# Kernel optimization log

Measured on AMD Instinct MI355X. Metric: run time of the kernel, lower is better.

The kernel has to match this reference:

```python
import jax, jax.numpy as jnp
import numpy as np

V, C, H, L, BLK = 32000, 1024, 16, 4, 1024
B, T = 4, 1024
FF = 100
HD = C // H
EPS = 1e-5


def setup_inputs() -> dict:
    key = jax.random.key(0)
    ks = jax.random.split(key, 16)
    n = lambda k, s: (jax.random.normal(k, s, dtype=jnp.float32) * 0.02)
    inp = {
        "idx": jax.random.randint(ks[0], (B, T), 0, V),
        "tok_emb": n(ks[1], (V, C)),
        "pos_emb": n(ks[2], (BLK, C)),
        "Wq": n(ks[3], (L, C, C)), "bq": jnp.zeros((L, C)),
        "Wk": n(ks[4], (L, C, C)), "bk": jnp.zeros((L, C)),
        "Wv": n(ks[5], (L, C, C)), "bv": jnp.zeros((L, C)),
        "Wo": n(ks[6], (L, C, C)), "bo": jnp.zeros((L, C)),
        "ln1_w": jnp.ones((L, C)), "ln1_b": jnp.zeros((L, C)),
        "ln2_w": jnp.ones((L, C)), "ln2_b": jnp.zeros((L, C)),
        "W1": n(ks[7], (L, C, FF)), "b1": jnp.zeros((L, FF)),
        "W2": n(ks[8], (L, FF, C)), "b2": jnp.zeros((L, C)),
        "lnf_w": jnp.ones((C,)), "lnf_b": jnp.zeros((C,)),
    }
    return inp


def _ln(x, w, b):
    m = jnp.mean(x, -1, keepdims=True)
    v = jnp.mean(jnp.square(x - m), -1, keepdims=True)
    return (x - m) * jax.lax.rsqrt(v + EPS) * w + b


def reference(idx, tok_emb, pos_emb, Wq, bq, Wk, bk, Wv, bv, Wo, bo,
              ln1_w, ln1_b, ln2_w, ln2_b, W1, b1, W2, b2, lnf_w, lnf_b):
    Bn, Tn = idx.shape
    x = tok_emb[idx] + pos_emb[:Tn][None]  # [B,T,C]; dropout is identity at eval
    scale = 1.0 / np.sqrt(HD).astype(np.float32)
    att_maps = []
    for l in range(L):
        h = _ln(x, ln1_w[l], ln1_b[l])
        q = (h @ Wq[l] + bq[l]).reshape(Bn, Tn, H, HD).transpose(0, 2, 1, 3)
        k = (h @ Wk[l] + bk[l]).reshape(Bn, Tn, H, HD).transpose(0, 2, 1, 3)
        v = (h @ Wv[l] + bv[l]).reshape(Bn, Tn, H, HD).transpose(0, 2, 1, 3)
        att = jax.nn.softmax(jnp.einsum("bhqd,bhkd->bhqk", q, k) * scale, axis=-1)
        y = jnp.einsum("bhqk,bhkd->bhqd", att, v).transpose(0, 2, 1, 3).reshape(Bn, Tn, C)
        x = x + (y @ Wo[l] + bo[l])
        f = _ln(x, ln2_w[l], ln2_b[l])
        f = jax.nn.relu(f @ W1[l] + b1[l]) @ W2[l] + b2[l]
        x = x + f
        att_maps.append(att.mean(0))  # [H,T,T]
    x = _ln(x, lnf_w, lnf_b)
    pooled = x.mean(1)  # [B,C]
    return pooled, jnp.stack(att_maps)  # [L,H,T,T]
```

## Files before the change

kernel.cpp:

```cpp
#include <hip/hip_runtime.h>

typedef __bf16 bf16;
typedef __bf16 bf16x4 __attribute__((ext_vector_type(4)));
typedef __bf16 bf16x8 __attribute__((ext_vector_type(8)));
typedef float  f32x4  __attribute__((ext_vector_type(4)));

static constexpr int kC   = 1024;
static constexpr int kT   = 1024;
static constexpr int kB   = 4;
static constexpr int kH   = 16;
static constexpr int kHD  = 64;
static constexpr int kL   = 4;
static constexpr int kFF  = 100;
static constexpr int kFFP = 128;
static constexpr int kM   = kB * kT;

__device__ __forceinline__ void gload16(const bf16* g, bf16* l)
{
    __builtin_amdgcn_global_load_lds(
        (const __attribute__((address_space(1))) void*)g,
        (__attribute__((address_space(3))) void*)l, 16, 0, 0);
}

__device__ __forceinline__ unsigned bpack(float a, float b)
{
    bf16 x = (bf16)a, y = (bf16)b;
    unsigned short ux = __builtin_bit_cast(unsigned short, x);
    unsigned short uy = __builtin_bit_cast(unsigned short, y);
    return (unsigned)ux | ((unsigned)uy << 16);
}
__device__ __forceinline__ float blo(unsigned u) { return __builtin_bit_cast(float, u << 16); }
__device__ __forceinline__ float bhi(unsigned u) { return __builtin_bit_cast(float, u & 0xffff0000u); }

__global__ __launch_bounds__(256)
void prep_kernel(const float* __restrict__ Wq, const float* __restrict__ Wk,
                 const float* __restrict__ Wv, const float* __restrict__ Wo,
                 const float* __restrict__ W1, const float* __restrict__ W2,
                 const float* __restrict__ bq, const float* __restrict__ bk,
                 const float* __restrict__ bv,
                 bf16* __restrict__ WQKVT, bf16* __restrict__ WOT,
                 bf16* __restrict__ W1T, bf16* __restrict__ W2T,
                 float* __restrict__ BQKV, float* __restrict__ pooled)
{
    __shared__ float tile[32][33];
    const int bid = blockIdx.x, tid = threadIdx.x;
    const float* src; bf16* dst; int K, N, KP, NP, bx, by;
    if (bid < 12288) {
        const int slab = bid >> 10, within = bid & 1023;
        const int l = slab / 3, which = slab % 3;
        const float* W = (which == 0) ? Wq : (which == 1) ? Wk : Wv;
        src = W + (long)l * kC * kC;
        dst = WQKVT + (long)l * 3 * kC * kC + (long)which * kC * kC;
        K = N = KP = NP = kC; bx = within & 31; by = within >> 5;
    } else if (bid < 16384) {
        const int t = bid - 12288, z = t >> 10, within = t & 1023;
        src = Wo + (long)z * kC * kC; dst = WOT + (long)z * kC * kC;
        K = N = KP = NP = kC; bx = within & 31; by = within >> 5;
    } else if (bid < 16896) {
        const int t = bid - 16384, z = t >> 7, within = t & 127;
        src = W1 + (long)z * kC * kFF; dst = W1T + (long)z * kFFP * kC;
        K = kC; N = kFF; KP = kC; NP = kFFP; bx = within & 3; by = within >> 2;
    } else if (bid < 17408) {
        const int t = bid - 16896, z = t >> 7, within = t & 127;
        src = W2 + (long)z * kFF * kC; dst = W2T + (long)z * kC * kFFP;
        K = kFF; N = kC; KP = kFFP; NP = kC; bx = within & 31; by = within >> 5;
    } else if (bid < 17456) {
        const int gid = (bid - 17408) * 256 + tid;
        const int l = gid / (3 * kC), wq = (gid / kC) % 3, c = gid & (kC - 1);
        const float* s = (wq == 0) ? bq : (wq == 1) ? bk : bv;
        BQKV[gid] = s[l * kC + c];
        return;
    } else {
        const int i = (bid - 17456) * 256 + tid;
        if (i < kB * kC) pooled[i] = 0.f;
        return;
    }
    const int n0 = bx * 32, k0 = by * 32;
    const int tx = tid & 31, ty = tid >> 5;
#pragma unroll
    for (int i = 0; i < 4; ++i) {
        int k = k0 + ty + i * 8, n = n0 + tx;
        tile[ty + i * 8][tx] = (k < K && n < N) ? src[(long)k * N + n] : 0.f;
    }
    __syncthreads();
#pragma unroll
    for (int i = 0; i < 4; ++i) {
        int n = n0 + ty + i * 8, k = k0 + tx;
        if (n < NP && k < KP) dst[(long)n * KP + k] = (bf16)tile[tx][ty + i * 8];
    }
}

__global__ __launch_bounds__(256)
void embed_kernel(const int* __restrict__ idx, const float* __restrict__ tok,
                  const float* __restrict__ pos, float* __restrict__ x)
{
    const int m = blockIdx.x;
    const int c = threadIdx.x * 4;
    const int t = m & (kT - 1);
    const long tk = (long)idx[m] * kC;
    float4 a = *(const float4*)&tok[tk + c];
    float4 b = *(const float4*)&pos[(long)t * kC + c];
    float4 o; o.x = a.x + b.x; o.y = a.y + b.y; o.z = a.z + b.z; o.w = a.w + b.w;
    *(float4*)&x[(long)m * kC + c] = o;
}

__global__ __launch_bounds__(256)
void ln_kernel(const float* __restrict__ x, const float* __restrict__ g,
               const float* __restrict__ be, bf16* __restrict__ ob)
{
    __shared__ float red[8];
    const long row = blockIdx.x;
    const int tid = threadIdx.x, lane = tid & 63, wv = tid >> 6;
    const float4 v = *(const float4*)&x[row * kC + tid * 4];
    float s = v.x + v.y + v.z + v.w;
    float s2 = v.x * v.x + v.y * v.y + v.z * v.z + v.w * v.w;
#pragma unroll
    for (int o = 32; o > 0; o >>= 1) { s += __shfl_down(s, o); s2 += __shfl_down(s2, o); }
    if (!lane) { red[wv] = s; red[4 + wv] = s2; }
    __syncthreads();
    s  = red[0] + red[1] + red[2] + red[3];
    s2 = red[4] + red[5] + red[6] + red[7];
    const float mean = s * (1.f / kC);
    const float var  = s2 * (1.f / kC) - mean * mean;
    const float rstd = rsqrtf(var + 1e-5f);
    const float4 gg = *(const float4*)&g[tid * 4];
    const float4 bb = *(const float4*)&be[tid * 4];
    bf16x4 o;
    o[0] = (bf16)((v.x - mean) * rstd * gg.x + bb.x);
    o[1] = (bf16)((v.y - mean) * rstd * gg.y + bb.y);
    o[2] = (bf16)((v.z - mean) * rstd * gg.z + bb.z);
    o[3] = (bf16)((v.w - mean) * rstd * gg.w + bb.w);
    *(bf16x4*)&ob[row * kC + tid * 4] = o;
}

template<int WAVES_M, int WAVES_N, int AI, int BJ, int MODE, int GL>
__global__ __launch_bounds__(256)
void gemm_bf16(const bf16* __restrict__ Ag, long strideA,
               const bf16* __restrict__ Bg, long strideB,
               const float* __restrict__ bias, int strideBias,
               bf16* __restrict__ outb, long strideOut,
               float* __restrict__ resid,
               int N, int K, int lda, int ldb)
{
    constexpr int BM = WAVES_M * AI * 16;
    constexpr int BN = WAVES_N * BJ * 16;
    constexpr int BK = 64;
    constexpr int LK = GL ? BK : (BK + 8);
    __shared__ __align__(16) bf16 As[BM * LK];
    __shared__ __align__(16) bf16 Bs[BN * LK];
    const int tid = threadIdx.x, lane = tid & 63, wv = tid >> 6;
    const int wm = wv / WAVES_N, wn = wv % WAVES_N;
    const int lr = lane & 15, lg = lane >> 4;
    const int z = blockIdx.z;
    const bf16* A = Ag + (long)z * strideA;
    const bf16* B = Bg + (long)z * strideB;
    const float* bi = bias ? bias + (long)z * strideBias : nullptr;
    const int m0 = blockIdx.y * BM, n0 = blockIdx.x * BN;

    f32x4 acc[AI][BJ];
#pragma unroll
    for (int i = 0; i < AI; ++i)
#pragma unroll
        for (int j = 0; j < BJ; ++j) acc[i][j] = (f32x4){0.f, 0.f, 0.f, 0.f};

    for (int k0 = 0; k0 < K; k0 += BK) {
        if constexpr (GL) {
            static_assert(BM == 128 && BN == 128, "GL path needs 128x128 tile");
            const int srow = wv * 32 + (lane >> 3);
            const int gcb  = (lane & 7) ^ (lane >> 3);
#pragma unroll
            for (int p = 0; p < 4; ++p) {
                gload16(A + (long)(m0 + srow + p * 8) * lda + k0 + gcb * 8,
                        &As[(wv * 32 + p * 8) * BK]);
                gload16(B + (long)(n0 + srow + p * 8) * ldb + k0 + gcb * 8,
                        &Bs[(wv * 32 + p * 8) * BK]);
            }
        } else {
            constexpr int AP = (BM * BK) / (256 * 8);
#pragma unroll
            for (int p = 0; p < AP; ++p) {
                int r = p * 32 + (tid >> 3), c = (tid & 7) * 8;
                *(uint4*)&As[r * LK + c] = *(const uint4*)&A[(long)(m0 + r) * lda + k0 + c];
            }
            constexpr int BP = (BN * BK) / (256 * 8);
#pragma unroll
            for (int p = 0; p < BP; ++p) {
                int r = p * 32 + (tid >> 3), c = (tid & 7) * 8;
                *(uint4*)&Bs[r * LK + c] = *(const uint4*)&B[(long)(n0 + r) * ldb + k0 + c];
            }
        }
        __syncthreads();
#pragma unroll
        for (int kk = 0; kk < 2; ++kk) {
            bf16x8 af[AI], bfv[BJ];
#pragma unroll
            for (int i = 0; i < AI; ++i) {
                const int r = wm * AI * 16 + i * 16 + lr;
                const int c = GL ? (((kk * 4 + lg) ^ (lr & 7)) * 8) : (kk * 32 + lg * 8);
                af[i] = *(const bf16x8*)&As[r * LK + c];
            }
#pragma unroll
            for (int j = 0; j < BJ; ++j) {
                const int r = wn * BJ * 16 + j * 16 + lr;
                const int c = GL ? (((kk * 4 + lg) ^ (lr & 7)) * 8) : (kk * 32 + lg * 8);
                bfv[j] = *(const bf16x8*)&Bs[r * LK + c];
            }
#pragma unroll
            for (int i = 0; i < AI; ++i)
#pragma unroll
                for (int j = 0; j < BJ; ++j)
                    acc[i][j] = __builtin_amdgcn_mfma_f32_16x16x32_bf16(af[i], bfv[j], acc[i][j], 0, 0, 0);
        }
        __syncthreads();
    }

#pragma unroll
    for (int i = 0; i < AI; ++i)
#pragma unroll
        for (int j = 0; j < BJ; ++j)
#pragma unroll
            for (int rr = 0; rr < 4; ++rr) {
                const int grow = m0 + wm * AI * 16 + i * 16 + lg * 4 + rr;
                const int gcol = n0 + wn * BJ * 16 + j * 16 + lr;
                float v = acc[i][j][rr];
                if constexpr (MODE == 0) {
                    v += bi[gcol];
                    if (z == 0) v *= 0.125f * 1.44269504f;
                    const int b = grow >> 10, t = grow & (kT - 1);
                    const int hh = gcol >> 6, hd = gcol & 63;
                    long o = (long)z * strideOut;
                    if (z == 2) o += (((long)b * kH + hh) * kHD + hd) * kT + t;
                    else        o += (((long)b * kH + hh) * kT + t) * kHD + hd;
                    outb[o] = (bf16)v;
                } else {
                    v += bi[gcol];
                    resid[(long)grow * N + gcol] += v;
                }
            }
}

__global__ __launch_bounds__(256, 2)
void ff_fused(float* __restrict__ X, const float* __restrict__ g,
              const float* __restrict__ be,
              const bf16* __restrict__ W1T_, const float* __restrict__ b1_,
              const bf16* __restrict__ W2T_, const float* __restrict__ b2_)
{
    __shared__ __align__(16) bf16 Hs[16 * kC];
    __shared__ __align__(16) bf16 F1s[16 * kFFP];
    const int tid = threadIdx.x, lane = tid & 63, w = tid >> 6;
    const int lr = lane & 15, lg = lane >> 4;
    const int r0 = blockIdx.x * 16;

    {
        const int row = tid >> 4, c16 = tid & 15;
        float4 xv[16];
        float s1 = 0.f, s2 = 0.f;
#pragma unroll
        for (int p = 0; p < 8; ++p) {
            const float* base = &X[(long)(r0 + row) * kC + p * 128 + c16 * 8];
            xv[2 * p]     = *(const float4*)base;
            xv[2 * p + 1] = *(const float4*)(base + 4);
#pragma unroll
            for (int e = 0; e < 4; ++e) {
                float a0 = ((const float*)&xv[2 * p])[e], a1 = ((const float*)&xv[2 * p + 1])[e];
                s1 += a0 + a1; s2 += a0 * a0 + a1 * a1;
            }
        }
#pragma unroll
        for (int off = 1; off < 16; off <<= 1) { s1 += __shfl_xor(s1, off); s2 += __shfl_xor(s2, off); }
        const float mean = s1 * (1.f / kC);
        const float rstd = rsqrtf(s2 * (1.f / kC) - mean * mean + 1e-5f);
#pragma unroll
        for (int p = 0; p < 8; ++p) {
            const int c0 = p * 128 + c16 * 8;
            float4 g0 = *(const float4*)&g[c0],  g1 = *(const float4*)&g[c0 + 4];
            float4 b0 = *(const float4*)&be[c0], b1v = *(const float4*)&be[c0 + 4];
            float h[8];
#pragma unroll
            for (int e = 0; e < 4; ++e) {
                h[e]     = (((const float*)&xv[2 * p])[e]     - mean) * rstd * ((const float*)&g0)[e] + ((const float*)&b0)[e];
                h[4 + e] = (((const float*)&xv[2 * p + 1])[e] - mean) * rstd * ((const float*)&g1)[e] + ((const float*)&b1v)[e];
            }
            uint4 hv;
            hv.x = bpack(h[0], h[1]); hv.y = bpack(h[2], h[3]);
            hv.z = bpack(h[4], h[5]); hv.w = bpack(h[6], h[7]);
            const int cb = c16 + p * 16;
            *(uint4*)&Hs[row * kC + ((cb ^ (row & 7)) << 3)] = hv;
        }
    }
    __syncthreads();

    {
        f32x4 accA[2], accB[2];
#pragma unroll
        for (int j = 0; j < 2; ++j) { accA[j] = (f32x4){0,0,0,0}; accB[j] = (f32x4){0,0,0,0}; }
        for (int k0 = 0; k0 < kC; k0 += 64) {
            const bf16x8 a0 = *(const bf16x8*)&Hs[lr * kC + ((((k0 >> 3) + 0 * 4 + lg) ^ (lr & 7)) << 3)];
            const bf16x8 a1 = *(const bf16x8*)&Hs[lr * kC + ((((k0 >> 3) + 1 * 4 + lg) ^ (lr & 7)) << 3)];
#pragma unroll
            for (int j = 0; j < 2; ++j) {
                const bf16x8 b0 = *(const bf16x8*)&W1T_[(long)(w * 32 + j * 16 + lr) * kC + k0 + 0 * 32 + lg * 8];
                const bf16x8 b1 = *(const bf16x8*)&W1T_[(long)(w * 32 + j * 16 + lr) * kC + k0 + 1 * 32 + lg * 8];
                accA[j] = __builtin_amdgcn_mfma_f32_16x16x32_bf16(a0, b0, accA[j], 0, 0, 0);
                accB[j] = __builtin_amdgcn_mfma_f32_16x16x32_bf16(a1, b1, accB[j], 0, 0, 0);
            }
        }
#pragma unroll
        for (int j = 0; j < 2; ++j)
#pragma unroll
            for (int rr = 0; rr < 4; ++rr) {
                const int row = lg * 4 + rr, col = w * 32 + j * 16 + lr;
                float v = accA[j][rr] + accB[j][rr] + (col < kFF ? b1_[col] : 0.f);
                F1s[row * kFFP + (((col >> 3) ^ (row & 7)) << 3) + (col & 7)] = (bf16)fmaxf(v, 0.f);
            }
    }
    __syncthreads();

    for (int nc = 0; nc < 8; ++nc) {
        f32x4 acc[2];
        acc[0] = (f32x4){0.f, 0.f, 0.f, 0.f};
        acc[1] = (f32x4){0.f, 0.f, 0.f, 0.f};
#pragma unroll
        for (int kk = 0; kk < 4; ++kk) {
            const bf16x8 a = *(const bf16x8*)&F1s[lr * kFFP + (((kk * 4 + lg) ^ (lr & 7)) << 3)];
#pragma unroll
            for (int j = 0; j < 2; ++j) {
                const bf16x8 bv = *(const bf16x8*)&W2T_[(long)(nc * 128 + w * 32 + j * 16 + lr) * kFFP + kk * 32 + lg * 8];
                acc[j] = __builtin_amdgcn_mfma_f32_16x16x32_bf16(a, bv, acc[j], 0, 0, 0);
            }
        }
#pragma unroll
        for (int j = 0; j < 2; ++j)
#pragma unroll
            for (int rr = 0; rr < 4; ++rr) {
                const int row = r0 + lg * 4 + rr, col = nc * 128 + w * 32 + j * 16 + lr;
                X[(long)row * kC + col] += acc[j][rr] + b2_[col];
            }
    }
}

__global__ __launch_bounds__(512, 2)
void attn_fused(const bf16* __restrict__ Qg, const bf16* __restrict__ Kg,
                const bf16* __restrict__ VTg, bf16* __restrict__ yg,
                float* __restrict__ attm)
{
    __shared__ __align__(16) bf16 Ps[32 * kT];
    __shared__ float reds[32][8];
    __shared__ float invs[32];
    const int tid = threadIdx.x, lane = tid & 63, w = tid >> 6;
    const int lr = lane & 15, lg = lane >> 4;
    const int bid = blockIdx.x, r_ = bid >> 3;
    const int h = ((bid & 7) << 1) | (r_ & 1);
    const int q0 = (r_ >> 1) * 32;
    const int rh = w >> 2, ch = w & 3;

    const int tbB = w * 16 + (lg >> 1);
    const int loB = (lg & 1) * 4;
    unsigned am_[2][4][2][2];
#pragma unroll
    for (int hf = 0; hf < 2; ++hf)
#pragma unroll
        for (int j = 0; j < 4; ++j)
#pragma unroll
            for (int qt = 0; qt < 2; ++qt)
#pragma unroll
                for (int d = 0; d < 2; ++d) am_[hf][j][qt][d] = 0u;

    for (int b = 0; b < kB; ++b) {
        const long bh = (long)b * kH + h;
        const bf16* Qb = Qg + (bh * kT + q0) * kHD;
        const bf16* Kb = Kg + bh * kT * kHD;
        const bf16* Vb = VTg + bh * (long)kHD * kT;

        if (b) __syncthreads();

        bf16x8 qf[2][2];
#pragma unroll
        for (int qt = 0; qt < 2; ++qt)
#pragma unroll
            for (int kk = 0; kk < 2; ++kk)
                qf[qt][kk] = *(const bf16x8*)&Qb[(qt * 16 + lr) * kHD + kk * 32 + lg * 8];

        float s[2] = {0.f, 0.f};

#pragma unroll
        for (int hf = 0; hf < 2; ++hf) {
            f32x4 acc[4][2];
#pragma unroll
            for (int j = 0; j < 4; ++j)
#pragma unroll
                for (int qt = 0; qt < 2; ++qt) acc[j][qt] = (f32x4){0.f, 0.f, 0.f, 0.f};
            __builtin_amdgcn_s_setprio(1);
#pragma unroll
            for (int j = 0; j < 4; ++j) {
                const int trow = w * 128 + hf * 64 + j * 16 + lr;
#pragma unroll
                for (int kk = 0; kk < 2; ++kk) {
                    const bf16x8 kf = *(const bf16x8*)&Kb[trow * kHD + kk * 32 + lg * 8];
                    acc[j][0] = __builtin_amdgcn_mfma_f32_16x16x32_bf16(kf, qf[0][kk], acc[j][0], 0, 0, 0);
                    acc[j][1] = __builtin_amdgcn_mfma_f32_16x16x32_bf16(kf, qf[1][kk], acc[j][1], 0, 0, 0);
                }
            }
            __builtin_amdgcn_s_setprio(0);
#pragma unroll
            for (int j = 0; j < 4; ++j) {
                const int tb = tbB + hf * 8 + j * 2;
#pragma unroll
                for (int qt = 0; qt < 2; ++qt) {
                    float e0 = exp2f(acc[j][qt][0]);
                    float e1 = exp2f(acc[j][qt][1]);
                    float e2 = exp2f(acc[j][qt][2]);
                    float e3 = exp2f(acc[j][qt][3]);
                    s[qt] += (e0 + e1) + (e2 + e3);
                    const int q = qt * 16 + lr;
                    uint2 pk; pk.x = bpack(e0, e1); pk.y = bpack(e2, e3);
                    *(uint2*)&Ps[q * kT + ((tb ^ (q & 7)) << 3) + loB] = pk;
                }
            }
        }

#pragma unroll
        for (int qt = 0; qt < 2; ++qt) {
            s[qt] += __shfl_xor(s[qt], 16);
            s[qt] += __shfl_xor(s[qt], 32);
        }
        if (lane < 16) { reds[lane][w] = s[0]; reds[16 + lane][w] = s[1]; }
        __syncthreads();

        float inv[2], iv4[2];
#pragma unroll
        for (int qt = 0; qt < 2; ++qt) {
            const int q = qt * 16 + lr;
            float4 a = *(const float4*)&reds[q][0];
            float4 c = *(const float4*)&reds[q][4];
            float tot = ((a.x + a.y) + (a.z + a.w)) + ((c.x + c.y) + (c.z + c.w));
            inv[qt] = __builtin_amdgcn_rcpf(tot);
            iv4[qt] = inv[qt] * 0.25f;
        }
        if (lane < 16) { invs[lane] = inv[0]; invs[16 + lane] = inv[1]; }

#pragma unroll
        for (int hf = 0; hf < 2; ++hf)
#pragma unroll
            for (int j = 0; j < 4; ++j) {
                const int tb = tbB + hf * 8 + j * 2;
#pragma unroll
                for (int qt = 0; qt < 2; ++qt) {
                    const int q = qt * 16 + lr;
                    uint2 e2 = *(const uint2*)&Ps[q * kT + ((tb ^ (q & 7)) << 3) + loB];
#pragma unroll
                    for (int d = 0; d < 2; ++d) {
                        unsigned ev = d ? e2.y : e2.x;
                        unsigned av = am_[hf][j][qt][d];
                        float n0 = blo(av) + blo(ev) * iv4[qt];
                        float n1 = bhi(av) + bhi(ev) * iv4[qt];
                        am_[hf][j][qt][d] = bpack(n0, n1);
                    }
                }
            }

        f32x4 yacc0 = (f32x4){0.f, 0.f, 0.f, 0.f};
        f32x4 yacc1 = (f32x4){0.f, 0.f, 0.f, 0.f};
        const int rowA = rh * 16 + lr;
        const int dRow = (ch * 16 + lr) * kT;
        __builtin_amdgcn_s_setprio(1);
#pragma unroll 4
        for (int kb = 0; kb < 32; kb += 2) {
            const bf16x8 a0 = *(const bf16x8*)&Ps[rowA * kT + (((kb * 4 + lg) ^ (rowA & 7)) << 3)];
            const bf16x8 v0 = *(const bf16x8*)&Vb[dRow + kb * 32 + lg * 8];
            const bf16x8 a1 = *(const bf16x8*)&Ps[rowA * kT + ((((kb + 1) * 4 + lg) ^ (rowA & 7)) << 3)];
            const bf16x8 v1 = *(const bf16x8*)&Vb[dRow + (kb + 1) * 32 + lg * 8];
            yacc0 = __builtin_amdgcn_mfma_f32_16x16x32_bf16(a0, v0, yacc0, 0, 0, 0);
            yacc1 = __builtin_amdgcn_mfma_f32_16x16x32_bf16(a1, v1, yacc1, 0, 0, 0);
        }
        __builtin_amdgcn_s_setprio(0);
#pragma unroll
        for (int rr = 0; rr < 4; ++rr) {
            const float iv = invs[rh * 16 + lg * 4 + rr];
            yg[((long)b * kT + q0 + rh * 16 + lg * 4 + rr) * kC + h * kHD + ch * 16 + lr]
                = (bf16)((yacc0[rr] + yacc1[rr]) * iv);
        }
    }

    __syncthreads();
    float* amf = (float*)Ps;
#pragma unroll
    for (int th = 0; th < 2; ++th) {
        if ((w >> 2) == th) {
#pragma unroll
            for (int hf = 0; hf < 2; ++hf)
#pragma unroll
                for (int j = 0; j < 4; ++j) {
                    const int tl = (w & 3) * 128 + hf * 64 + j * 16 + lg * 4;
#pragma unroll
                    for (int qt = 0; qt < 2; ++qt) {
                        const int q = qt * 16 + lr;
#pragma unroll
                        for (int d = 0; d < 2; ++d) {
                            unsigned av = am_[hf][j][qt][d];
                            amf[q * 512 + tl + 2 * d]     = blo(av);
                            amf[q * 512 + tl + 2 * d + 1] = bhi(av);
                        }
                    }
                }
        }
        __syncthreads();
#pragma unroll
        for (int p = 0; p < 8; ++p) {
            const int f = p * 512 + tid;
            const int row = f >> 7, c4 = f & 127;
            float4 v = *(const float4*)&amf[row * 512 + c4 * 4];
            *(float4*)&attm[((long)h * kT + q0 + row) * kT + th * 512 + c4 * 4] = v;
        }
        __syncthreads();
    }
}

__global__ __launch_bounds__(256)
void pool_kernel(const bf16* __restrict__ hb, float* __restrict__ pooled)
{
    const int c = blockIdx.x * 256 + threadIdx.x;
    const int b = blockIdx.y;
    const int t0 = blockIdx.z * 128;
    float s = 0.f;
    for (int t = t0; t < t0 + 128; ++t) s += (float)hb[((long)b * kT + t) * kC + c];
    atomicAdd(&pooled[b * kC + c], s * (1.f / kT));
}

extern "C" void kernel_launch(void* const* d_in, const int* in_sizes, int n_in,
                              void* d_out, int out_size, void* d_ws, size_t ws_size,
                              hipStream_t stream)
{
    const int*   idx  = (const int*)d_in[0];
    const float* tok  = (const float*)d_in[1];
    const float* pos  = (const float*)d_in[2];
    const float* Wq   = (const float*)d_in[3];
    const float* bq   = (const float*)d_in[4];
    const float* Wk   = (const float*)d_in[5];
    const float* bk   = (const float*)d_in[6];
    const float* Wv   = (const float*)d_in[7];
    const float* bv   = (const float*)d_in[8];
    const float* Wo   = (const float*)d_in[9];
    const float* bo   = (const float*)d_in[10];
    const float* ln1w = (const float*)d_in[11];
    const float* ln1b = (const float*)d_in[12];
    const float* ln2w = (const float*)d_in[13];
    const float* ln2b = (const float*)d_in[14];
    const float* W1   = (const float*)d_in[15];
    const float* b1   = (const float*)d_in[16];
    const float* W2   = (const float*)d_in[17];
    const float* b2   = (const float*)d_in[18];
    const float* lnfw = (const float*)d_in[19];
    const float* lnfb = (const float*)d_in[20];

    char* ws = (char*)d_ws;
    long off = 0;
    auto alloc = [&](long bytes) { char* p = ws + off; off += (bytes + 255) & ~255L; return p; };
    bf16*  WQKVT = (bf16*)alloc((long)kL * 3 * kC * kC * 2);
    bf16*  WOT   = (bf16*)alloc((long)kL * kC * kC * 2);
    bf16*  W1T   = (bf16*)alloc((long)kL * kFFP * kC * 2);
    bf16*  W2T   = (bf16*)alloc((long)kL * kC * kFFP * 2);
    float* BQKV  = (float*)alloc((long)kL * 3 * kC * 4);
    float* X     = (float*)alloc((long)kM * kC * 4);
    bf16*  Hbuf  = (bf16*)alloc((long)kM * kC * 2);
    bf16*  QKV   = (bf16*)alloc(3L * kM * kC * 2);
    bf16*  Y     = (bf16*)alloc((long)kM * kC * 2);

    float* pooled = (float*)d_out;
    float* attm_base = pooled + kB * kC;

    prep_kernel<<<17472, 256, 0, stream>>>(Wq, Wk, Wv, Wo, W1, W2, bq, bk, bv,
                                           WQKVT, WOT, W1T, W2T, BQKV, pooled);
    embed_kernel<<<kM, 256, 0, stream>>>(idx, tok, pos, X);

    for (int l = 0; l < kL; ++l) {
        ln_kernel<<<kM, 256, 0, stream>>>(X, ln1w + l * kC, ln1b + l * kC, Hbuf);
        gemm_bf16<2, 2, 4, 4, 0, 1><<<dim3(8, 32, 3), 256, 0, stream>>>(
            Hbuf, 0L, WQKVT + (long)l * 3 * kC * kC, (long)kC * kC,
            BQKV + l * 3 * kC, kC, QKV, (long)kM * kC, nullptr,
            kC, kC, kC, kC);
        attn_fused<<<dim3(512), 512, 0, stream>>>(
            QKV, QKV + (long)kM * kC, QKV + 2L * kM * kC, Y,
            attm_base + (long)l * kH * kT * kT);
        gemm_bf16<2, 2, 4, 4, 4, 1><<<dim3(8, 32, 1), 256, 0, stream>>>(
            Y, 0L, WOT + (long)l * kC * kC, 0L, bo + l * kC, 0,
            nullptr, 0L, X, kC, kC, kC, kC);
        ff_fused<<<256, 256, 0, stream>>>(X, ln2w + l * kC, ln2b + l * kC,
                                          W1T + (long)l * kFFP * kC, b1 + l * kFF,
                                          W2T + (long)l * kC * kFFP, b2 + l * kC);
    }
    ln_kernel<<<kM, 256, 0, stream>>>(X, lnfw, lnfb, Hbuf);
    pool_kernel<<<dim3(4, kB, 8), 256, 0, stream>>>(Hbuf, pooled);
}
```

Before: 980.2 us.

## Shrink attention blocks to 16 queries with 4 waves and split Wo GEMM rows

Attention now launches 1024 blocks of 256 threads, each handling 16 query rows instead of 32. Each wave covers 256 keys and one 16-wide head-dim slice of V. This halves the shared-memory probability buffer and allows more blocks per CU, aiming for better occupancy and load balance. The cost is that K and V are re-read twice as often across blocks. The output-projection GEMM also switches to a 64x128 tile with twice as many row blocks, and the global-load-to-LDS path is generalized to support that tile shape.

```diff
diff --git a/kernel.cpp b/kernel.cpp
--- a/kernel.cpp
+++ b/kernel.cpp
@@ -165,16 +165,19 @@
 
     for (int k0 = 0; k0 < K; k0 += BK) {
         if constexpr (GL) {
-            static_assert(BM == 128 && BN == 128, "GL path needs 128x128 tile");
-            const int srow = wv * 32 + (lane >> 3);
-            const int gcb  = (lane & 7) ^ (lane >> 3);
-#pragma unroll
-            for (int p = 0; p < 4; ++p) {
-                gload16(A + (long)(m0 + srow + p * 8) * lda + k0 + gcb * 8,
-                        &As[(wv * 32 + p * 8) * BK]);
-                gload16(B + (long)(n0 + srow + p * 8) * ldb + k0 + gcb * 8,
-                        &Bs[(wv * 32 + p * 8) * BK]);
-            }
+            static_assert((BM % 32) == 0 && (BN % 32) == 0, "GL tile multiple of 32");
+            const int sr  = lane >> 3;
+            const int gcb = (lane & 7) ^ sr;
+            constexpr int ARW = BM / 4;
+            constexpr int BRW = BN / 4;
+#pragma unroll
+            for (int p = 0; p < BM / 32; ++p)
+                gload16(A + (long)(m0 + wv * ARW + p * 8 + sr) * lda + k0 + gcb * 8,
+                        &As[(wv * ARW + p * 8) * BK]);
+#pragma unroll
+            for (int p = 0; p < BN / 32; ++p)
+                gload16(B + (long)(n0 + wv * BRW + p * 8 + sr) * ldb + k0 + gcb * 8,
+                        &Bs[(wv * BRW + p * 8) * BK]);
         } else {
             constexpr int AP = (BM * BK) / (256 * 8);
 #pragma unroll
@@ -339,32 +342,29 @@
     }
 }
 
-__global__ __launch_bounds__(512, 2)
+__global__ __launch_bounds__(256, 4)
 void attn_fused(const bf16* __restrict__ Qg, const bf16* __restrict__ Kg,
                 const bf16* __restrict__ VTg, bf16* __restrict__ yg,
                 float* __restrict__ attm)
 {
-    __shared__ __align__(16) bf16 Ps[32 * kT];
-    __shared__ float reds[32][8];
-    __shared__ float invs[32];
+    __shared__ __align__(16) bf16 Ps[16 * kT];
+    __shared__ __align__(16) float reds[16][4];
+    __shared__ float invs[16];
     const int tid = threadIdx.x, lane = tid & 63, w = tid >> 6;
     const int lr = lane & 15, lg = lane >> 4;
     const int bid = blockIdx.x, r_ = bid >> 3;
     const int h = ((bid & 7) << 1) | (r_ & 1);
-    const int q0 = (r_ >> 1) * 32;
-    const int rh = w >> 2, ch = w & 3;
-
-    const int tbB = w * 16 + (lg >> 1);
+    const int q0 = (r_ >> 1) * 16;
+
+    const int tbB = w * 32 + (lg >> 1);
     const int loB = (lg & 1) * 4;
-    unsigned am_[2][4][2][2];
+    unsigned am_[2][8][2];
 #pragma unroll
     for (int hf = 0; hf < 2; ++hf)
 #pragma unroll
-        for (int j = 0; j < 4; ++j)
-#pragma unroll
-            for (int qt = 0; qt < 2; ++qt)
-#pragma unroll
-                for (int d = 0; d < 2; ++d) am_[hf][j][qt][d] = 0u;
+        for (int j = 0; j < 8; ++j)
+#pragma unroll
+            for (int d = 0; d < 2; ++d) am_[hf][j][d] = 0u;
 
     for (int b = 0; b < kB; ++b) {
         const long bh = (long)b * kH + h;
@@ -374,111 +374,86 @@
 
         if (b) __syncthreads();
 
-        bf16x8 qf[2][2];
-#pragma unroll
-        for (int qt = 0; qt < 2; ++qt)
-#pragma unroll
-            for (int kk = 0; kk < 2; ++kk)
-                qf[qt][kk] = *(const bf16x8*)&Qb[(qt * 16 + lr) * kHD + kk * 32 + lg * 8];
-
-        float s[2] = {0.f, 0.f};
-
+        bf16x8 qf[2];
+#pragma unroll
+        for (int kk = 0; kk < 2; ++kk)
+            qf[kk] = *(const bf16x8*)&Qb[lr * kHD + kk * 32 + lg * 8];
+
+        float s = 0.f;
 #pragma unroll
         for (int hf = 0; hf < 2; ++hf) {
-            f32x4 acc[4][2];
-#pragma unroll
-            for (int j = 0; j < 4; ++j)
-#pragma unroll
-                for (int qt = 0; qt < 2; ++qt) acc[j][qt] = (f32x4){0.f, 0.f, 0.f, 0.f};
+            f32x4 acc[8];
+#pragma unroll
+            for (int j = 0; j < 8; ++j) acc[j] = (f32x4){0.f, 0.f, 0.f, 0.f};
             __builtin_amdgcn_s_setprio(1);
 #pragma unroll
-            for (int j = 0; j < 4; ++j) {
-                const int trow = w * 128 + hf * 64 + j * 16 + lr;
+            for (int j = 0; j < 8; ++j) {
+                const int trow = w * 256 + hf * 128 + j * 16 + lr;
 #pragma unroll
                 for (int kk = 0; kk < 2; ++kk) {
                     const bf16x8 kf = *(const bf16x8*)&Kb[trow * kHD + kk * 32 + lg * 8];
-                    acc[j][0] = __builtin_amdgcn_mfma_f32_16x16x32_bf16(kf, qf[0][kk], acc[j][0], 0, 0, 0);
-                    acc[j][1] = __builtin_amdgcn_mfma_f32_16x16x32_bf16(kf, qf[1][kk], acc[j][1], 0, 0, 0);
+                    acc[j] = __builtin_amdgcn_mfma_f32_16x16x32_bf16(kf, qf[kk], acc[j], 0, 0, 0);
                 }
             }
             __builtin_amdgcn_s_setprio(0);
 #pragma unroll
-            for (int j = 0; j < 4; ++j) {
-                const int tb = tbB + hf * 8 + j * 2;
-#pragma unroll
-                for (int qt = 0; qt < 2; ++qt) {
-                    float e0 = exp2f(acc[j][qt][0]);
-                    float e1 = exp2f(acc[j][qt][1]);
-                    float e2 = exp2f(acc[j][qt][2]);
-                    float e3 = exp2f(acc[j][qt][3]);
-                    s[qt] += (e0 + e1) + (e2 + e3);
-                    const int q = qt * 16 + lr;
-                    uint2 pk; pk.x = bpack(e0, e1); pk.y = bpack(e2, e3);
-                    *(uint2*)&Ps[q * kT + ((tb ^ (q & 7)) << 3) + loB] = pk;
+            for (int j = 0; j < 8; ++j) {
+                const int tb = tbB + hf * 16 + j * 2;
+                float e0 = exp2f(acc[j][0]);
+                float e1 = exp2f(acc[j][1]);
+                float e2 = exp2f(acc[j][2]);
+                float e3 = exp2f(acc[j][3]);
+                s += (e0 + e1) + (e2 + e3);
+                uint2 pk; pk.x = bpack(e0, e1); pk.y = bpack(e2, e3);
+                *(uint2*)&Ps[lr * kT + ((tb ^ (lr & 7)) << 3) + loB] = pk;
+            }
+        }
+
+        s += __shfl_xor(s, 16);
+        s += __shfl_xor(s, 32);
+        if (lane < 16) reds[lane][w] = s;
+        __syncthreads();
+
+        float4 rv = *(const float4*)&reds[lr][0];
+        const float inv = __builtin_amdgcn_rcpf((rv.x + rv.y) + (rv.z + rv.w));
+        const float iv4 = inv * 0.25f;
+        if (lane < 16) invs[lane] = inv;
+
+#pragma unroll
+        for (int hf = 0; hf < 2; ++hf)
+#pragma unroll
+            for (int j = 0; j < 8; ++j) {
+                const int tb = tbB + hf * 16 + j * 2;
+                uint2 e2 = *(const uint2*)&Ps[lr * kT + ((tb ^ (lr & 7)) << 3) + loB];
+#pragma unroll
+                for (int d = 0; d < 2; ++d) {
+                    unsigned ev = d ? e2.y : e2.x;
+                    unsigned av = am_[hf][j][d];
+                    float n0 = blo(av) + blo(ev) * iv4;
+                    float n1 = bhi(av) + bhi(ev) * iv4;
+                    am_[hf][j][d] = bpack(n0, n1);
                 }
             }
-        }
-
-#pragma unroll
-        for (int qt = 0; qt < 2; ++qt) {
-            s[qt] += __shfl_xor(s[qt], 16);
-            s[qt] += __shfl_xor(s[qt], 32);
-        }
-        if (lane < 16) { reds[lane][w] = s[0]; reds[16 + lane][w] = s[1]; }
-        __syncthreads();
-
-        float inv[2], iv4[2];
-#pragma unroll
-        for (int qt = 0; qt < 2; ++qt) {
-            const int q = qt * 16 + lr;
-            float4 a = *(const float4*)&reds[q][0];
-            float4 c = *(const float4*)&reds[q][4];
-            float tot = ((a.x + a.y) + (a.z + a.w)) + ((c.x + c.y) + (c.z + c.w));
-            inv[qt] = __builtin_amdgcn_rcpf(tot);
-            iv4[qt] = inv[qt] * 0.25f;
-        }
-        if (lane < 16) { invs[lane] = inv[0]; invs[16 + lane] = inv[1]; }
-
-#pragma unroll
-        for (int hf = 0; hf < 2; ++hf)
-#pragma unroll
-            for (int j = 0; j < 4; ++j) {
-                const int tb = tbB + hf * 8 + j * 2;
-#pragma unroll
-                for (int qt = 0; qt < 2; ++qt) {
-                    const int q = qt * 16 + lr;
-                    uint2 e2 = *(const uint2*)&Ps[q * kT + ((tb ^ (q & 7)) << 3) + loB];
-#pragma unroll
-                    for (int d = 0; d < 2; ++d) {
-                        unsigned ev = d ? e2.y : e2.x;
-                        unsigned av = am_[hf][j][qt][d];
-                        float n0 = blo(av) + blo(ev) * iv4[qt];
-                        float n1 = bhi(av) + bhi(ev) * iv4[qt];
-                        am_[hf][j][qt][d] = bpack(n0, n1);
-                    }
-                }
-            }
-
-        f32x4 yacc0 = (f32x4){0.f, 0.f, 0.f, 0.f};
-        f32x4 yacc1 = (f32x4){0.f, 0.f, 0.f, 0.f};
-        const int rowA = rh * 16 + lr;
-        const int dRow = (ch * 16 + lr) * kT;
+
+        f32x4 y0 = (f32x4){0.f, 0.f, 0.f, 0.f};
+        f32x4 y1 = (f32x4){0.f, 0.f, 0.f, 0.f};
+        const int vRow = (w * 16 + lr) * kT;
         __builtin_amdgcn_s_setprio(1);
 #pragma unroll 4
         for (int kb = 0; kb < 32; kb += 2) {
-            const bf16x8 a0 = *(const bf16x8*)&Ps[rowA * kT + (((kb * 4 + lg) ^ (rowA & 7)) << 3)];
-            const bf16x8 v0 = *(const bf16x8*)&Vb[dRow + kb * 32 + lg * 8];
-            const bf16x8 a1 = *(const bf16x8*)&Ps[rowA * kT + ((((kb + 1) * 4 + lg) ^ (rowA & 7)) << 3)];
-            const bf16x8 v1 = *(const bf16x8*)&Vb[dRow + (kb + 1) * 32 + lg * 8];
-            yacc0 = __builtin_amdgcn_mfma_f32_16x16x32_bf16(a0, v0, yacc0, 0, 0, 0);
-            yacc1 = __builtin_amdgcn_mfma_f32_16x16x32_bf16(a1, v1, yacc1, 0, 0, 0);
+            const bf16x8 a0 = *(const bf16x8*)&Ps[lr * kT + (((kb * 4 + lg) ^ (lr & 7)) << 3)];
+            const bf16x8 v0 = *(const bf16x8*)&Vb[vRow + kb * 32 + lg * 8];
+            const bf16x8 a1 = *(const bf16x8*)&Ps[lr * kT + ((((kb + 1) * 4 + lg) ^ (lr & 7)) << 3)];
+            const bf16x8 v1 = *(const bf16x8*)&Vb[vRow + (kb + 1) * 32 + lg * 8];
+            y0 = __builtin_amdgcn_mfma_f32_16x16x32_bf16(a0, v0, y0, 0, 0, 0);
+            y1 = __builtin_amdgcn_mfma_f32_16x16x32_bf16(a1, v1, y1, 0, 0, 0);
         }
         __builtin_amdgcn_s_setprio(0);
 #pragma unroll
         for (int rr = 0; rr < 4; ++rr) {
-            const float iv = invs[rh * 16 + lg * 4 + rr];
-            yg[((long)b * kT + q0 + rh * 16 + lg * 4 + rr) * kC + h * kHD + ch * 16 + lr]
-                = (bf16)((yacc0[rr] + yacc1[rr]) * iv);
+            const float iv = invs[lg * 4 + rr];
+            yg[((long)b * kT + q0 + lg * 4 + rr) * kC + h * kHD + w * 16 + lr]
+                = (bf16)((y0[rr] + y1[rr]) * iv);
         }
     }
 
@@ -486,28 +461,24 @@
     float* amf = (float*)Ps;
 #pragma unroll
     for (int th = 0; th < 2; ++th) {
-        if ((w >> 2) == th) {
+        if ((w >> 1) == th) {
 #pragma unroll
             for (int hf = 0; hf < 2; ++hf)
 #pragma unroll
-                for (int j = 0; j < 4; ++j) {
-                    const int tl = (w & 3) * 128 + hf * 64 + j * 16 + lg * 4;
-#pragma unroll
-                    for (int qt = 0; qt < 2; ++qt) {
-                        const int q = qt * 16 + lr;
-#pragma unroll
-                        for (int d = 0; d < 2; ++d) {
-                            unsigned av = am_[hf][j][qt][d];
-                            amf[q * 512 + tl + 2 * d]     = blo(av);
-                            amf[q * 512 + tl + 2 * d + 1] = bhi(av);
-                        }
+                for (int j = 0; j < 8; ++j) {
+                    const int tl = (w & 1) * 256 + hf * 128 + j * 16 + lg * 4;
+#pragma unroll
+                    for (int d = 0; d < 2; ++d) {
+                        unsigned av = am_[hf][j][d];
+                        amf[lr * 512 + tl + 2 * d]     = blo(av);
+                        amf[lr * 512 + tl + 2 * d + 1] = bhi(av);
                     }
                 }
         }
         __syncthreads();
 #pragma unroll
         for (int p = 0; p < 8; ++p) {
-            const int f = p * 512 + tid;
+            const int f = p * 256 + tid;
             const int row = f >> 7, c4 = f & 127;
             float4 v = *(const float4*)&amf[row * 512 + c4 * 4];
             *(float4*)&attm[((long)h * kT + q0 + row) * kT + th * 512 + c4 * 4] = v;
@@ -579,10 +550,10 @@
             Hbuf, 0L, WQKVT + (long)l * 3 * kC * kC, (long)kC * kC,
             BQKV + l * 3 * kC, kC, QKV, (long)kM * kC, nullptr,
             kC, kC, kC, kC);
-        attn_fused<<<dim3(512), 512, 0, stream>>>(
+        attn_fused<<<dim3(1024), 256, 0, stream>>>(
             QKV, QKV + (long)kM * kC, QKV + 2L * kM * kC, Y,
             attm_base + (long)l * kH * kT * kT);
-        gemm_bf16<2, 2, 4, 4, 4, 1><<<dim3(8, 32, 1), 256, 0, stream>>>(
+        gemm_bf16<2, 2, 2, 4, 4, 1><<<dim3(8, 64, 1), 256, 0, stream>>>(
             Y, 0L, WOT + (long)l * kC * kC, 0L, bo + l * kC, 0,
             nullptr, 0L, X, kC, kC, kC, kC);
         ff_fused<<<256, 256, 0, stream>>>(X, ln2w + l * kC, ln2b + l * kC,
```

New measurement: 1.037 ms. 5.8% more time.
